# Kernel optimization log

Hardware: AMD Instinct MI355X
Metric: run time of the kernel (lower is better)

The kernel has to match this reference:

```python
import jax, jax.numpy as jnp
import numpy as np

NEG = -10000000.0

def setup_inputs() -> dict:
    key0 = jax.random.key(0)
    ks = jax.random.split(key0, 5)
    B, XL, KL, D = 16, 1024, 512, 1024  # D = 2*rnn_dim
    return {
        "x": jax.random.normal(ks[0], (B, XL, D), dtype=jnp.float32),
        "x_mask": jnp.ones((B, XL), dtype=jnp.float32),
        "key": jax.random.normal(ks[1], (B, KL, D), dtype=jnp.float32),
        "key_mask": jnp.ones((B, KL), dtype=jnp.float32),
        "w_input": jax.random.normal(ks[2], (D,), dtype=jnp.float32) / np.sqrt(D),
        "w_key": jax.random.normal(ks[3], (D,), dtype=jnp.float32) / np.sqrt(D),
        "dot_w": jax.random.normal(ks[4], (D,), dtype=jnp.float32) / np.sqrt(D),
    }

def reference(x, x_mask, key, key_mask, w_input, w_key, dot_w):
    # Trilinear attention score S[b,i,j] = w_in.x_i + w_key.k_j + (x_i*dot_w).k_j
    x_logits = jnp.einsum('bxd,d->bx', x, w_input)      # [B, XL]
    key_logits = jnp.einsum('bkd,d->bk', key, w_key)    # [B, KL]
    S = (x_logits[:, :, None] + key_logits[:, None, :]
         + jnp.einsum('bxd,bkd->bxk', x * dot_w, key))  # [B, XL, KL]

    # x -> key attention with joint mask
    joint_mask = 1.0 - x_mask[:, :, None] * key_mask[:, None, :]
    masked_S = S + joint_mask * NEG
    attn = jax.nn.softmax(masked_S, axis=-1)
    x2key = jnp.einsum('bxk,bkd->bxd', attn, key)       # [B, XL, D]

    # key -> x attention: mask over key dim, max-reduce, masked softmax over x
    km = key_mask[:, None, :]
    S2 = S * km + (1.0 - km) * NEG                      # add_masked_value
    max_s = jnp.max(S2, axis=-1)                        # [B, XL]
    p = jax.nn.softmax(max_s * x_mask, axis=-1) * x_mask  # claf masked_softmax
    p = p / (jnp.sum(p, axis=-1, keepdims=True) + 1e-13)
    key2x = jnp.einsum('bx,bxd->bd', p, x)[:, None, :]  # [B, 1, D], broadcasts

    key2x_full = jnp.broadcast_to(key2x, x.shape)
    return jnp.concatenate([x, x2key, x * x2key, x * key2x_full], axis=-1)
```

## Files before the change

### kernel.cpp

```cpp
#include <hip/hip_runtime.h>
#include <hip/hip_fp16.h>

#define B_ 16
#define XL_ 1024
#define KL_ 512
#define D_ 1024
#define NEGC (-10000000.0f)

typedef _Float16 f16x8 __attribute__((ext_vector_type(8)));
typedef float f32x4 __attribute__((ext_vector_type(4)));
typedef unsigned short u16x8 __attribute__((ext_vector_type(8)));
typedef unsigned short u16x4 __attribute__((ext_vector_type(4)));

__device__ __forceinline__ unsigned short f2h(float f) {
  __half h = __float2half(f);
  return __half_as_ushort(h);
}

__global__ __launch_bounds__(256) void k_build(const float* __restrict__ key,
    const float* __restrict__ w_key, unsigned short* __restrict__ KQ2,
    unsigned short* __restrict__ KV2, float* __restrict__ klog) {
  __shared__ unsigned short tile[64][72];
  int bid = blockIdx.x;
  int b = bid >> 4;
  int ks = (bid >> 1) & 7;
  int dh = bid & 1;
  int tid = threadIdx.x;
  int kr = tid >> 2;
  int cq = tid & 3;
  const float* krow = key + ((size_t)(b * KL_ + ks * 64 + kr)) * D_;
  float klacc = 0.f;
  int dl = tid & 63, g = tid >> 6;

  for (int dt = dh * 8; dt < dh * 8 + 8; ++dt) {
#pragma unroll
    for (int j = 0; j < 4; ++j) {
      int c = dt * 64 + cq * 16 + j * 4;
      f32x4 v = __builtin_nontemporal_load((const f32x4*)(krow + c));
      f32x4 w = *(const f32x4*)(w_key + c);
      klacc += v[0] * w[0] + v[1] * w[1] + v[2] * w[2] + v[3] * w[3];
      u16x4 hv;
      hv[0] = f2h(v[0]); hv[1] = f2h(v[1]); hv[2] = f2h(v[2]); hv[3] = f2h(v[3]);
      *(u16x4*)(&tile[kr][cq * 16 + j * 4]) = hv;
    }
    __syncthreads();
#pragma unroll
    for (int dkc_l = 0; dkc_l < 2; ++dkc_l) {
      u16x8 hv = *(const u16x8*)(&tile[kr][dkc_l * 32 + cq * 8]);
      size_t dst = (((size_t)(b * 8 + ks) * 32 + (dt * 2 + dkc_l)) << 11)
                   + (size_t)(((kr >> 4) & 3) * 512 + (cq * 16 + (kr & 15)) * 8);
      *(u16x8*)(KQ2 + dst) = hv;
    }
    {
      int dglob = dt * 64 + dl;
      int wv_ = dglob >> 7, np = (dglob >> 4) & 7, l15v = dglob & 15;
#pragma unroll
      for (int kkc_l = 0; kkc_l < 2; ++kkc_l) {
        u16x8 hv;
#pragma unroll
        for (int h = 0; h < 8; ++h) hv[h] = tile[kkc_l * 32 + g * 8 + h][dl];
        size_t dst = (((size_t)(b * 8 + wv_) * 16 + (ks * 2 + kkc_l)) << 12)
                     + (size_t)(np * 512 + (g * 16 + l15v) * 8);
        *(u16x8*)(KV2 + dst) = hv;
      }
    }
    __syncthreads();
  }
  klacc += __shfl_xor(klacc, 1);
  klacc += __shfl_xor(klacc, 2);
  if (cq == 0) atomicAdd(&klog[b * KL_ + ks * 64 + kr], klacc);
}

__global__ __launch_bounds__(512, 4) void k_attn(
    const float* __restrict__ x, const float* __restrict__ x_mask,
    const float* __restrict__ key_mask, const float* __restrict__ dot_w,
    const float* __restrict__ w_input,
    const unsigned short* __restrict__ KQ2, const unsigned short* __restrict__ KV2,
    const float* __restrict__ klog,
    float* __restrict__ maxs, float* __restrict__ out) {
  __shared__ unsigned short Qall[32 * 1024];
  __shared__ float xlg[32];
  unsigned short* Pt = Qall;
  float* redA = (float*)(Qall + 16384);
  float* redB = redA + 256;
  float* redC = redB + 256;

  const int tid = threadIdx.x;
  const int wv = tid >> 6;
  const int lane = tid & 63;
  const int l15 = lane & 15, l4 = lane >> 4;
  const int r7 = l15 & 7;

  int bid = blockIdx.x;
  int b = (bid & 7) * 2 + (bid >> 8);
  int x0 = ((bid >> 3) & 31) * 32;

  const float* xB = x + ((size_t)b * XL_ + x0) * D_;

  {
    int row = tid >> 4;
    int cg = tid & 15;
    const float* sp = xB + (size_t)row * D_;
    char* qrow = (char*)Qall + row * 2048;
    int rsw = row & 7;
    float xl = 0.f;
#pragma unroll
    for (int j = 0; j < 16; ++j) {
      int c4 = cg + j * 16;
      f32x4 v = *(const f32x4*)(sp + c4 * 4);
      f32x4 w = *(const f32x4*)(dot_w + c4 * 4);
      f32x4 wi = *(const f32x4*)(w_input + c4 * 4);
      xl += v[0] * wi[0] + v[1] * wi[1] + v[2] * wi[2] + v[3] * wi[3];
      u16x4 hv;
      hv[0] = f2h(v[0] * w[0]); hv[1] = f2h(v[1] * w[1]);
      hv[2] = f2h(v[2] * w[2]); hv[3] = f2h(v[3] * w[3]);
      *(u16x4*)(qrow + (((c4 >> 1) ^ rsw) << 4) + ((c4 & 1) << 3)) = hv;
    }
    xl += __shfl_xor(xl, 1);
    xl += __shfl_xor(xl, 2);
    xl += __shfl_xor(xl, 4);
    xl += __shfl_xor(xl, 8);
    if (cg == 0) xlg[row] = xl;
  }
  __syncthreads();

  f32x4 acc[2][4];
#pragma unroll
  for (int m = 0; m < 2; ++m)
#pragma unroll
    for (int n = 0; n < 4; ++n) { f32x4 z = {0.f, 0.f, 0.f, 0.f}; acc[m][n] = z; }

  const unsigned short* KQ2w = KQ2 + (((size_t)(b * 8 + wv) * 32) << 11) + lane * 8;
  const char* qa0 = (char*)Qall + l15 * 2048;
  const char* qa1 = (char*)Qall + (16 + l15) * 2048;

#pragma unroll 4
  for (int dk = 0; dk < D_; dk += 32) {
    const unsigned short* cp = KQ2w + ((dk >> 5) << 11);
    f16x8 b0 = *(const f16x8*)(cp);
    f16x8 b1 = *(const f16x8*)(cp + 512);
    f16x8 b2 = *(const f16x8*)(cp + 1024);
    f16x8 b3 = *(const f16x8*)(cp + 1536);
    int c = (((dk >> 3) + l4) ^ r7) << 4;
    f16x8 a0 = *(const f16x8*)(qa0 + c);
    f16x8 a1 = *(const f16x8*)(qa1 + c);
    __builtin_amdgcn_s_setprio(1);
    acc[0][0] = __builtin_amdgcn_mfma_f32_16x16x32_f16(b0, a0, acc[0][0], 0, 0, 0);
    acc[1][0] = __builtin_amdgcn_mfma_f32_16x16x32_f16(b0, a1, acc[1][0], 0, 0, 0);
    acc[0][1] = __builtin_amdgcn_mfma_f32_16x16x32_f16(b1, a0, acc[0][1], 0, 0, 0);
    acc[1][1] = __builtin_amdgcn_mfma_f32_16x16x32_f16(b1, a1, acc[1][1], 0, 0, 0);
    acc[0][2] = __builtin_amdgcn_mfma_f32_16x16x32_f16(b2, a0, acc[0][2], 0, 0, 0);
    acc[1][2] = __builtin_amdgcn_mfma_f32_16x16x32_f16(b2, a1, acc[1][2], 0, 0, 0);
    acc[0][3] = __builtin_amdgcn_mfma_f32_16x16x32_f16(b3, a0, acc[0][3], 0, 0, 0);
    acc[1][3] = __builtin_amdgcn_mfma_f32_16x16x32_f16(b3, a1, acc[1][3], 0, 0, 0);
    __builtin_amdgcn_s_setprio(0);
  }
  __syncthreads();

  float xlv[2], xmv[2];
#pragma unroll
  for (int m = 0; m < 2; ++m) {
    int row = m * 16 + l15;
    xlv[m] = xlg[row];
    xmv[m] = x_mask[(size_t)b * XL_ + x0 + row];
  }
  f32x4 klv[4], kmv[4];
#pragma unroll
  for (int n = 0; n < 4; ++n) {
    int kb = wv * 64 + n * 16 + l4 * 4;
    klv[n] = *(const f32x4*)(klog + (size_t)b * KL_ + kb);
    kmv[n] = *(const f32x4*)(key_mask + (size_t)b * KL_ + kb);
  }
  float mxsm[2] = {-3.0e38f, -3.0e38f}, mxs2[2] = {-3.0e38f, -3.0e38f};
#pragma unroll
  for (int m = 0; m < 2; ++m)
#pragma unroll
    for (int n = 0; n < 4; ++n)
#pragma unroll
      for (int q = 0; q < 4; ++q) {
        float s = acc[m][n][q] + xlv[m] + klv[n][q];
        float sm = s + (1.f - xmv[m] * kmv[n][q]) * NEGC;
        float s2 = s * kmv[n][q] + (1.f - kmv[n][q]) * NEGC;
        mxsm[m] = fmaxf(mxsm[m], sm);
        mxs2[m] = fmaxf(mxs2[m], s2);
      }
#pragma unroll
  for (int m = 0; m < 2; ++m) {
    mxsm[m] = fmaxf(mxsm[m], __shfl_xor(mxsm[m], 16));
    mxsm[m] = fmaxf(mxsm[m], __shfl_xor(mxsm[m], 32));
    mxs2[m] = fmaxf(mxs2[m], __shfl_xor(mxs2[m], 16));
    mxs2[m] = fmaxf(mxs2[m], __shfl_xor(mxs2[m], 32));
  }
  if (l4 == 0) {
#pragma unroll
    for (int m = 0; m < 2; ++m) {
      redA[wv * 32 + m * 16 + l15] = mxsm[m];
      redB[wv * 32 + m * 16 + l15] = mxs2[m];
    }
  }
  __syncthreads();
  float gmx[2];
#pragma unroll
  for (int m = 0; m < 2; ++m) {
    int row = m * 16 + l15;
    float v = redA[row];
#pragma unroll
    for (int w = 1; w < 8; ++w) v = fmaxf(v, redA[w * 32 + row]);
    gmx[m] = v;
  }
  if (tid < 32) {
    float v = redB[tid];
#pragma unroll
    for (int w = 1; w < 8; ++w) v = fmaxf(v, redB[w * 32 + tid]);
    maxs[(size_t)b * XL_ + x0 + tid] = v;
  }
  float rs[2] = {0.f, 0.f};
#pragma unroll
  for (int m = 0; m < 2; ++m) {
    int row = m * 16 + l15;
    char* prow = (char*)Pt + row * 1024;
    int rsw = row & 7;
#pragma unroll
    for (int n = 0; n < 4; ++n) {
      int k = wv * 64 + n * 16 + l4 * 4;
      u16x4 pk;
#pragma unroll
      for (int q = 0; q < 4; ++q) {
        float s = acc[m][n][q] + xlv[m] + klv[n][q];
        float sm = s + (1.f - xmv[m] * kmv[n][q]) * NEGC;
        float e = __expf(sm - gmx[m]);
        rs[m] += e;
        pk[q] = f2h(e);
      }
      *(u16x4*)(prow + ((((k >> 3) ^ rsw) << 4) + ((k & 4) << 1))) = pk;
    }
  }
#pragma unroll
  for (int m = 0; m < 2; ++m) {
    rs[m] += __shfl_xor(rs[m], 16);
    rs[m] += __shfl_xor(rs[m], 32);
  }
  if (l4 == 0) {
#pragma unroll
    for (int m = 0; m < 2; ++m) redC[wv * 32 + m * 16 + l15] = rs[m];
  }
  __syncthreads();

  float dn[2];
#pragma unroll
  for (int m = 0; m < 2; ++m) {
    int row = m * 16 + l15;
    float sum = redC[row];
#pragma unroll
    for (int w = 1; w < 8; ++w) sum += redC[w * 32 + row];
    dn[m] = 1.f / sum;
  }
  size_t obase0 = ((size_t)b * XL_ + x0) * (size_t)(4 * D_);
  const char* pa0 = (char*)Pt + l15 * 1024;
  const char* pa1 = (char*)Pt + (16 + l15) * 1024;
  const unsigned short* KV2w = KV2 + (((size_t)(b * 8 + wv) * 16) << 12) + lane * 8;
#pragma unroll
  for (int sc = 0; sc < 2; ++sc) {
    int c0 = wv * 128 + sc * 64;
    f32x4 acc2[2][4];
#pragma unroll
    for (int m = 0; m < 2; ++m)
#pragma unroll
      for (int n = 0; n < 4; ++n) { f32x4 z = {0.f, 0.f, 0.f, 0.f}; acc2[m][n] = z; }
    const unsigned short* KV2s = KV2w + sc * 4 * 512;
#pragma unroll 4
    for (int kk = 0; kk < KL_; kk += 32) {
      const unsigned short* cp = KV2s + ((kk >> 5) << 12);
      f16x8 b0 = *(const f16x8*)(cp);
      f16x8 b1 = *(const f16x8*)(cp + 512);
      f16x8 b2 = *(const f16x8*)(cp + 1024);
      f16x8 b3 = *(const f16x8*)(cp + 1536);
      int c = ((((kk >> 3) + l4) ^ r7) << 4);
      f16x8 a0 = *(const f16x8*)(pa0 + c);
      f16x8 a1 = *(const f16x8*)(pa1 + c);
      __builtin_amdgcn_s_setprio(1);
      acc2[0][0] = __builtin_amdgcn_mfma_f32_16x16x32_f16(b0, a0, acc2[0][0], 0, 0, 0);
      acc2[1][0] = __builtin_amdgcn_mfma_f32_16x16x32_f16(b0, a1, acc2[1][0], 0, 0, 0);
      acc2[0][1] = __builtin_amdgcn_mfma_f32_16x16x32_f16(b1, a0, acc2[0][1], 0, 0, 0);
      acc2[1][1] = __builtin_amdgcn_mfma_f32_16x16x32_f16(b1, a1, acc2[1][1], 0, 0, 0);
      acc2[0][2] = __builtin_amdgcn_mfma_f32_16x16x32_f16(b2, a0, acc2[0][2], 0, 0, 0);
      acc2[1][2] = __builtin_amdgcn_mfma_f32_16x16x32_f16(b2, a1, acc2[1][2], 0, 0, 0);
      acc2[0][3] = __builtin_amdgcn_mfma_f32_16x16x32_f16(b3, a0, acc2[0][3], 0, 0, 0);
      acc2[1][3] = __builtin_amdgcn_mfma_f32_16x16x32_f16(b3, a1, acc2[1][3], 0, 0, 0);
      __builtin_amdgcn_s_setprio(0);
    }
#pragma unroll
    for (int m = 0; m < 2; ++m) {
      int row = m * 16 + l15;
      size_t ob = obase0 + (size_t)row * (4 * D_);
#pragma unroll
      for (int n = 0; n < 4; ++n) {
        int col = c0 + n * 16 + l4 * 4;
        f32x4 v = acc2[m][n];
        v[0] *= dn[m]; v[1] *= dn[m]; v[2] *= dn[m]; v[3] *= dn[m];
        __builtin_nontemporal_store(v, (f32x4*)(out + ob + D_ + col));
      }
    }
  }
}

__global__ __launch_bounds__(256) void k_key2x_part(const float* __restrict__ x,
    const float* __restrict__ maxs, const float* __restrict__ x_mask,
    float* __restrict__ partial) {
  int b = blockIdx.x >> 4;
  int xc = blockIdx.x & 15;
  int tid = threadIdx.x;
  int wvi = tid >> 6, lane = tid & 63;
  __shared__ float r1[4], r2[4], r3[4];
  __shared__ float ps_all[XL_];
  const float* ms = maxs + (size_t)b * XL_;
  const float* xm = x_mask + (size_t)b * XL_;
  float tv[4], xmv[4];
  float vmax = -3.0e38f;
#pragma unroll
  for (int i = 0; i < 4; ++i) {
    int xi = i * 256 + tid;
    xmv[i] = xm[xi];
    tv[i] = ms[xi] * xmv[i];
    vmax = fmaxf(vmax, tv[i]);
  }
#pragma unroll
  for (int sh = 32; sh >= 1; sh >>= 1) vmax = fmaxf(vmax, __shfl_xor(vmax, sh));
  if (lane == 0) r1[wvi] = vmax;
  __syncthreads();
  float gmax = fmaxf(fmaxf(r1[0], r1[1]), fmaxf(r1[2], r1[3]));
  float e[4]; float es = 0.f;
#pragma unroll
  for (int i = 0; i < 4; ++i) { e[i] = __expf(tv[i] - gmax); es += e[i]; }
#pragma unroll
  for (int sh = 32; sh >= 1; sh >>= 1) es += __shfl_xor(es, sh);
  if (lane == 0) r2[wvi] = es;
  __syncthreads();
  float gsum = r2[0] + r2[1] + r2[2] + r2[3];
  float pv4[4]; float psum = 0.f;
#pragma unroll
  for (int i = 0; i < 4; ++i) { pv4[i] = e[i] / gsum * xmv[i]; psum += pv4[i]; }
#pragma unroll
  for (int sh = 32; sh >= 1; sh >>= 1) psum += __shfl_xor(psum, sh);
  if (lane == 0) r3[wvi] = psum;
  __syncthreads();
  float gps = r3[0] + r3[1] + r3[2] + r3[3];
  float inv = 1.f / (gps + 1e-13f);
#pragma unroll
  for (int i = 0; i < 4; ++i) ps_all[i * 256 + tid] = pv4[i] * inv;
  __syncthreads();
  const float* xb = x + ((size_t)b * XL_ + xc * 64) * D_;
  float acc0 = 0.f, acc1 = 0.f, acc2 = 0.f, acc3 = 0.f;
  int d = tid;
  const float* psl = ps_all + xc * 64;
  for (int xi = 0; xi < 64; ++xi) {
    float pv = psl[xi];
    const float* rp = xb + (size_t)xi * D_;
    acc0 += pv * __builtin_nontemporal_load(rp + d);
    acc1 += pv * __builtin_nontemporal_load(rp + d + 256);
    acc2 += pv * __builtin_nontemporal_load(rp + d + 512);
    acc3 += pv * __builtin_nontemporal_load(rp + d + 768);
  }
  float* pp = partial + (size_t)blockIdx.x * D_;
  pp[d] = acc0; pp[d + 256] = acc1; pp[d + 512] = acc2; pp[d + 768] = acc3;
}

__global__ __launch_bounds__(256) void k_key2x_red(const float* __restrict__ partial,
    float* __restrict__ k2x) {
  int idx = blockIdx.x * 256 + threadIdx.x;
  int b = idx >> 10;
  float s = 0.f;
#pragma unroll
  for (int xc = 0; xc < 16; ++xc)
    s += partial[((size_t)b * 16 + xc) * D_ + (idx & 1023)];
  k2x[idx] = s;
}

__global__ __launch_bounds__(256) void k_mega(const float* __restrict__ x,
    const float* __restrict__ k2x, float* __restrict__ out) {
  size_t t = (size_t)blockIdx.x * 256 + threadIdx.x;
  size_t base = t * 4;
  int b = (int)(base >> 20);
  int rem = (int)(base & ((1u << 20) - 1));
  int xr = rem >> 10;
  int d = rem & 1023;
  f32x4 xv = __builtin_nontemporal_load((const f32x4*)(x + base));
  f32x4 kv = *(const f32x4*)(k2x + (size_t)b * D_ + d);
  float* orow = out + ((size_t)b * XL_ + xr) * (size_t)(4 * D_);
  f32x4 x2 = __builtin_nontemporal_load((const f32x4*)(orow + D_ + d));
  __builtin_nontemporal_store(xv, (f32x4*)(orow + d));
  f32x4 p2;
  p2[0] = xv[0] * x2[0]; p2[1] = xv[1] * x2[1];
  p2[2] = xv[2] * x2[2]; p2[3] = xv[3] * x2[3];
  __builtin_nontemporal_store(p2, (f32x4*)(orow + 2 * D_ + d));
  f32x4 p3;
  p3[0] = xv[0] * kv[0]; p3[1] = xv[1] * kv[1];
  p3[2] = xv[2] * kv[2]; p3[3] = xv[3] * kv[3];
  __builtin_nontemporal_store(p3, (f32x4*)(orow + 3 * D_ + d));
}

extern "C" void kernel_launch(void* const* d_in, const int* in_sizes, int n_in,
                              void* d_out, int out_size, void* d_ws, size_t ws_size,
                              hipStream_t stream) {
  (void)in_sizes; (void)n_in; (void)out_size; (void)ws_size;
  const float* x        = (const float*)d_in[0];
  const float* x_mask   = (const float*)d_in[1];
  const float* key      = (const float*)d_in[2];
  const float* key_mask = (const float*)d_in[3];
  const float* w_input  = (const float*)d_in[4];
  const float* w_key    = (const float*)d_in[5];
  const float* dot_w    = (const float*)d_in[6];
  float* out = (float*)d_out;
  char* ws = (char*)d_ws;

  unsigned short* KQ2 = (unsigned short*)ws;
  unsigned short* KV2 = (unsigned short*)(ws + (16u << 20));
  float* xlog = (float*)(ws + (32u << 20));
  float* klog = xlog + B_ * XL_;
  float* maxs = klog + B_ * KL_;
  float* pbuf = maxs + B_ * XL_;
  float* k2x  = pbuf + B_ * XL_;
  float* partial = (float*)ws;

  hipMemsetAsync(klog, 0, B_ * KL_ * sizeof(float), stream);
  k_build<<<dim3(B_ * 16), dim3(256), 0, stream>>>(key, w_key, KQ2, KV2, klog);
  k_attn<<<dim3(512), dim3(512), 0, stream>>>(x, x_mask, key_mask, dot_w, w_input,
                                              KQ2, KV2, klog, maxs, out);
  k_key2x_part<<<dim3(B_ * 16), dim3(256), 0, stream>>>(x, maxs, x_mask, partial);
  k_key2x_red<<<dim3(B_ * D_ / 256), dim3(256), 0, stream>>>(partial, k2x);
  k_mega<<<dim3(B_ * XL_ * D_ / 1024), dim3(256), 0, stream>>>(x, k2x, out);
}
```

Measured before the change: 169.1 us.

## Prefetch MFMA B-operands in registers and drop klog memset via partial sums

The QK and PV MFMA loops now double-buffer their global B-operand loads in registers, fetching the next 64-wide step while the current one computes. The first KQ2 and KV2 tiles are prefetched before the Q staging and the softmax epilogue, so their latency overlaps that work. k_build now splits D into four quarters across twice as many blocks and writes per-quarter key logits instead of using atomics. That removes the memset launch, and k_attn sums the four partials. The cost is higher register pressure under launch_bounds(512,4) and some extra klog reads.

```diff
diff --git a/kernel.cpp b/kernel.cpp
--- a/kernel.cpp
+++ b/kernel.cpp
@@ -19,12 +19,12 @@
 
 __global__ __launch_bounds__(256) void k_build(const float* __restrict__ key,
     const float* __restrict__ w_key, unsigned short* __restrict__ KQ2,
-    unsigned short* __restrict__ KV2, float* __restrict__ klog) {
+    unsigned short* __restrict__ KV2, float* __restrict__ klogP) {
   __shared__ unsigned short tile[64][72];
   int bid = blockIdx.x;
-  int b = bid >> 4;
-  int ks = (bid >> 1) & 7;
-  int dh = bid & 1;
+  int b = bid >> 5;
+  int ks = (bid >> 2) & 7;
+  int dq = bid & 3;
   int tid = threadIdx.x;
   int kr = tid >> 2;
   int cq = tid & 3;
@@ -32,7 +32,7 @@
   float klacc = 0.f;
   int dl = tid & 63, g = tid >> 6;
 
-  for (int dt = dh * 8; dt < dh * 8 + 8; ++dt) {
+  for (int dt = dq * 4; dt < dq * 4 + 4; ++dt) {
 #pragma unroll
     for (int j = 0; j < 4; ++j) {
       int c = dt * 64 + cq * 16 + j * 4;
@@ -68,7 +68,7 @@
   }
   klacc += __shfl_xor(klacc, 1);
   klacc += __shfl_xor(klacc, 2);
-  if (cq == 0) atomicAdd(&klog[b * KL_ + ks * 64 + kr], klacc);
+  if (cq == 0) klogP[(size_t)dq * (B_ * KL_) + b * KL_ + ks * 64 + kr] = klacc;
 }
 
 __global__ __launch_bounds__(512, 4) void k_attn(
@@ -76,7 +76,7 @@
     const float* __restrict__ key_mask, const float* __restrict__ dot_w,
     const float* __restrict__ w_input,
     const unsigned short* __restrict__ KQ2, const unsigned short* __restrict__ KV2,
-    const float* __restrict__ klog,
+    const float* __restrict__ klogP,
     float* __restrict__ maxs, float* __restrict__ out) {
   __shared__ unsigned short Qall[32 * 1024];
   __shared__ float xlg[32];
@@ -96,6 +96,16 @@
   int x0 = ((bid >> 3) & 31) * 32;
 
   const float* xB = x + ((size_t)b * XL_ + x0) * D_;
+  const unsigned short* KQ2w = KQ2 + (((size_t)(b * 8 + wv) * 32) << 11) + lane * 8;
+
+  f16x8 p00 = *(const f16x8*)(KQ2w);
+  f16x8 p01 = *(const f16x8*)(KQ2w + 512);
+  f16x8 p02 = *(const f16x8*)(KQ2w + 1024);
+  f16x8 p03 = *(const f16x8*)(KQ2w + 1536);
+  f16x8 p10 = *(const f16x8*)(KQ2w + 2048);
+  f16x8 p11 = *(const f16x8*)(KQ2w + 2048 + 512);
+  f16x8 p12 = *(const f16x8*)(KQ2w + 2048 + 1024);
+  f16x8 p13 = *(const f16x8*)(KQ2w + 2048 + 1536);
 
   {
     int row = tid >> 4;
@@ -130,32 +140,66 @@
 #pragma unroll
     for (int n = 0; n < 4; ++n) { f32x4 z = {0.f, 0.f, 0.f, 0.f}; acc[m][n] = z; }
 
-  const unsigned short* KQ2w = KQ2 + (((size_t)(b * 8 + wv) * 32) << 11) + lane * 8;
   const char* qa0 = (char*)Qall + l15 * 2048;
   const char* qa1 = (char*)Qall + (16 + l15) * 2048;
 
-#pragma unroll 4
-  for (int dk = 0; dk < D_; dk += 32) {
-    const unsigned short* cp = KQ2w + ((dk >> 5) << 11);
-    f16x8 b0 = *(const f16x8*)(cp);
-    f16x8 b1 = *(const f16x8*)(cp + 512);
-    f16x8 b2 = *(const f16x8*)(cp + 1024);
-    f16x8 b3 = *(const f16x8*)(cp + 1536);
-    int c = (((dk >> 3) + l4) ^ r7) << 4;
-    f16x8 a0 = *(const f16x8*)(qa0 + c);
-    f16x8 a1 = *(const f16x8*)(qa1 + c);
-    __builtin_amdgcn_s_setprio(1);
-    acc[0][0] = __builtin_amdgcn_mfma_f32_16x16x32_f16(b0, a0, acc[0][0], 0, 0, 0);
-    acc[1][0] = __builtin_amdgcn_mfma_f32_16x16x32_f16(b0, a1, acc[1][0], 0, 0, 0);
-    acc[0][1] = __builtin_amdgcn_mfma_f32_16x16x32_f16(b1, a0, acc[0][1], 0, 0, 0);
-    acc[1][1] = __builtin_amdgcn_mfma_f32_16x16x32_f16(b1, a1, acc[1][1], 0, 0, 0);
-    acc[0][2] = __builtin_amdgcn_mfma_f32_16x16x32_f16(b2, a0, acc[0][2], 0, 0, 0);
-    acc[1][2] = __builtin_amdgcn_mfma_f32_16x16x32_f16(b2, a1, acc[1][2], 0, 0, 0);
-    acc[0][3] = __builtin_amdgcn_mfma_f32_16x16x32_f16(b3, a0, acc[0][3], 0, 0, 0);
-    acc[1][3] = __builtin_amdgcn_mfma_f32_16x16x32_f16(b3, a1, acc[1][3], 0, 0, 0);
-    __builtin_amdgcn_s_setprio(0);
-  }
-  __syncthreads();
+#pragma unroll 2
+  for (int dk = 0; dk < D_; dk += 64) {
+    {
+      f16x8 b0 = p00, b1 = p01, b2 = p02, b3 = p03;
+      if (dk + 64 < D_) {
+        const unsigned short* cp = KQ2w + (((dk + 64) >> 5) << 11);
+        p00 = *(const f16x8*)(cp);
+        p01 = *(const f16x8*)(cp + 512);
+        p02 = *(const f16x8*)(cp + 1024);
+        p03 = *(const f16x8*)(cp + 1536);
+      }
+      int c = (((dk >> 3) + l4) ^ r7) << 4;
+      f16x8 a0 = *(const f16x8*)(qa0 + c);
+      f16x8 a1 = *(const f16x8*)(qa1 + c);
+      __builtin_amdgcn_s_setprio(1);
+      acc[0][0] = __builtin_amdgcn_mfma_f32_16x16x32_f16(b0, a0, acc[0][0], 0, 0, 0);
+      acc[1][0] = __builtin_amdgcn_mfma_f32_16x16x32_f16(b0, a1, acc[1][0], 0, 0, 0);
+      acc[0][1] = __builtin_amdgcn_mfma_f32_16x16x32_f16(b1, a0, acc[0][1], 0, 0, 0);
+      acc[1][1] = __builtin_amdgcn_mfma_f32_16x16x32_f16(b1, a1, acc[1][1], 0, 0, 0);
+      acc[0][2] = __builtin_amdgcn_mfma_f32_16x16x32_f16(b2, a0, acc[0][2], 0, 0, 0);
+      acc[1][2] = __builtin_amdgcn_mfma_f32_16x16x32_f16(b2, a1, acc[1][2], 0, 0, 0);
+      acc[0][3] = __builtin_amdgcn_mfma_f32_16x16x32_f16(b3, a0, acc[0][3], 0, 0, 0);
+      acc[1][3] = __builtin_amdgcn_mfma_f32_16x16x32_f16(b3, a1, acc[1][3], 0, 0, 0);
+      __builtin_amdgcn_s_setprio(0);
+    }
+    {
+      int dk2 = dk + 32;
+      f16x8 b0 = p10, b1 = p11, b2 = p12, b3 = p13;
+      if (dk2 + 64 < D_) {
+        const unsigned short* cp = KQ2w + (((dk2 + 64) >> 5) << 11);
+        p10 = *(const f16x8*)(cp);
+        p11 = *(const f16x8*)(cp + 512);
+        p12 = *(const f16x8*)(cp + 1024);
+        p13 = *(const f16x8*)(cp + 1536);
+      }
+      int c = (((dk2 >> 3) + l4) ^ r7) << 4;
+      f16x8 a0 = *(const f16x8*)(qa0 + c);
+      f16x8 a1 = *(const f16x8*)(qa1 + c);
+      __builtin_amdgcn_s_setprio(1);
+      acc[0][0] = __builtin_amdgcn_mfma_f32_16x16x32_f16(b0, a0, acc[0][0], 0, 0, 0);
+      acc[1][0] = __builtin_amdgcn_mfma_f32_16x16x32_f16(b0, a1, acc[1][0], 0, 0, 0);
+      acc[0][1] = __builtin_amdgcn_mfma_f32_16x16x32_f16(b1, a0, acc[0][1], 0, 0, 0);
+      acc[1][1] = __builtin_amdgcn_mfma_f32_16x16x32_f16(b1, a1, acc[1][1], 0, 0, 0);
+      acc[0][2] = __builtin_amdgcn_mfma_f32_16x16x32_f16(b2, a0, acc[0][2], 0, 0, 0);
+      acc[1][2] = __builtin_amdgcn_mfma_f32_16x16x32_f16(b2, a1, acc[1][2], 0, 0, 0);
+      acc[0][3] = __builtin_amdgcn_mfma_f32_16x16x32_f16(b3, a0, acc[0][3], 0, 0, 0);
+      acc[1][3] = __builtin_amdgcn_mfma_f32_16x16x32_f16(b3, a1, acc[1][3], 0, 0, 0);
+      __builtin_amdgcn_s_setprio(0);
+    }
+  }
+  __syncthreads();
+
+  const unsigned short* KV2w = KV2 + (((size_t)(b * 8 + wv) * 16) << 12) + lane * 8;
+  f16x8 v00 = *(const f16x8*)(KV2w);
+  f16x8 v01 = *(const f16x8*)(KV2w + 512);
+  f16x8 v02 = *(const f16x8*)(KV2w + 1024);
+  f16x8 v03 = *(const f16x8*)(KV2w + 1536);
 
   float xlv[2], xmv[2];
 #pragma unroll
@@ -168,7 +212,11 @@
 #pragma unroll
   for (int n = 0; n < 4; ++n) {
     int kb = wv * 64 + n * 16 + l4 * 4;
-    klv[n] = *(const f32x4*)(klog + (size_t)b * KL_ + kb);
+    f32x4 s0 = *(const f32x4*)(klogP + (size_t)b * KL_ + kb);
+    f32x4 s1 = *(const f32x4*)(klogP + (size_t)(B_ * KL_) + (size_t)b * KL_ + kb);
+    f32x4 s2 = *(const f32x4*)(klogP + (size_t)(2 * B_ * KL_) + (size_t)b * KL_ + kb);
+    f32x4 s3 = *(const f32x4*)(klogP + (size_t)(3 * B_ * KL_) + (size_t)b * KL_ + kb);
+    klv[n] = (s0 + s1) + (s2 + s3);
     kmv[n] = *(const f32x4*)(key_mask + (size_t)b * KL_ + kb);
   }
   float mxsm[2] = {-3.0e38f, -3.0e38f}, mxs2[2] = {-3.0e38f, -3.0e38f};
@@ -258,7 +306,6 @@
   size_t obase0 = ((size_t)b * XL_ + x0) * (size_t)(4 * D_);
   const char* pa0 = (char*)Pt + l15 * 1024;
   const char* pa1 = (char*)Pt + (16 + l15) * 1024;
-  const unsigned short* KV2w = KV2 + (((size_t)(b * 8 + wv) * 16) << 12) + lane * 8;
 #pragma unroll
   for (int sc = 0; sc < 2; ++sc) {
     int c0 = wv * 128 + sc * 64;
@@ -268,26 +315,67 @@
 #pragma unroll
       for (int n = 0; n < 4; ++n) { f32x4 z = {0.f, 0.f, 0.f, 0.f}; acc2[m][n] = z; }
     const unsigned short* KV2s = KV2w + sc * 4 * 512;
-#pragma unroll 4
-    for (int kk = 0; kk < KL_; kk += 32) {
-      const unsigned short* cp = KV2s + ((kk >> 5) << 12);
-      f16x8 b0 = *(const f16x8*)(cp);
-      f16x8 b1 = *(const f16x8*)(cp + 512);
-      f16x8 b2 = *(const f16x8*)(cp + 1024);
-      f16x8 b3 = *(const f16x8*)(cp + 1536);
-      int c = ((((kk >> 3) + l4) ^ r7) << 4);
-      f16x8 a0 = *(const f16x8*)(pa0 + c);
-      f16x8 a1 = *(const f16x8*)(pa1 + c);
-      __builtin_amdgcn_s_setprio(1);
-      acc2[0][0] = __builtin_amdgcn_mfma_f32_16x16x32_f16(b0, a0, acc2[0][0], 0, 0, 0);
-      acc2[1][0] = __builtin_amdgcn_mfma_f32_16x16x32_f16(b0, a1, acc2[1][0], 0, 0, 0);
-      acc2[0][1] = __builtin_amdgcn_mfma_f32_16x16x32_f16(b1, a0, acc2[0][1], 0, 0, 0);
-      acc2[1][1] = __builtin_amdgcn_mfma_f32_16x16x32_f16(b1, a1, acc2[1][1], 0, 0, 0);
-      acc2[0][2] = __builtin_amdgcn_mfma_f32_16x16x32_f16(b2, a0, acc2[0][2], 0, 0, 0);
-      acc2[1][2] = __builtin_amdgcn_mfma_f32_16x16x32_f16(b2, a1, acc2[1][2], 0, 0, 0);
-      acc2[0][3] = __builtin_amdgcn_mfma_f32_16x16x32_f16(b3, a0, acc2[0][3], 0, 0, 0);
-      acc2[1][3] = __builtin_amdgcn_mfma_f32_16x16x32_f16(b3, a1, acc2[1][3], 0, 0, 0);
-      __builtin_amdgcn_s_setprio(0);
+    f16x8 q00, q01, q02, q03, q10, q11, q12, q13;
+    if (sc == 0) { q00 = v00; q01 = v01; q02 = v02; q03 = v03; }
+    else {
+      q00 = *(const f16x8*)(KV2s);
+      q01 = *(const f16x8*)(KV2s + 512);
+      q02 = *(const f16x8*)(KV2s + 1024);
+      q03 = *(const f16x8*)(KV2s + 1536);
+    }
+    q10 = *(const f16x8*)(KV2s + 4096);
+    q11 = *(const f16x8*)(KV2s + 4096 + 512);
+    q12 = *(const f16x8*)(KV2s + 4096 + 1024);
+    q13 = *(const f16x8*)(KV2s + 4096 + 1536);
+#pragma unroll 2
+    for (int kk = 0; kk < KL_; kk += 64) {
+      {
+        f16x8 b0 = q00, b1 = q01, b2 = q02, b3 = q03;
+        if (kk + 64 < KL_) {
+          const unsigned short* cp = KV2s + (((kk + 64) >> 5) << 12);
+          q00 = *(const f16x8*)(cp);
+          q01 = *(const f16x8*)(cp + 512);
+          q02 = *(const f16x8*)(cp + 1024);
+          q03 = *(const f16x8*)(cp + 1536);
+        }
+        int c = ((((kk >> 3) + l4) ^ r7) << 4);
+        f16x8 a0 = *(const f16x8*)(pa0 + c);
+        f16x8 a1 = *(const f16x8*)(pa1 + c);
+        __builtin_amdgcn_s_setprio(1);
+        acc2[0][0] = __builtin_amdgcn_mfma_f32_16x16x32_f16(b0, a0, acc2[0][0], 0, 0, 0);
+        acc2[1][0] = __builtin_amdgcn_mfma_f32_16x16x32_f16(b0, a1, acc2[1][0], 0, 0, 0);
+        acc2[0][1] = __builtin_amdgcn_mfma_f32_16x16x32_f16(b1, a0, acc2[0][1], 0, 0, 0);
+        acc2[1][1] = __builtin_amdgcn_mfma_f32_16x16x32_f16(b1, a1, acc2[1][1], 0, 0, 0);
+        acc2[0][2] = __builtin_amdgcn_mfma_f32_16x16x32_f16(b2, a0, acc2[0][2], 0, 0, 0);
+        acc2[1][2] = __builtin_amdgcn_mfma_f32_16x16x32_f16(b2, a1, acc2[1][2], 0, 0, 0);
+        acc2[0][3] = __builtin_amdgcn_mfma_f32_16x16x32_f16(b3, a0, acc2[0][3], 0, 0, 0);
+        acc2[1][3] = __builtin_amdgcn_mfma_f32_16x16x32_f16(b3, a1, acc2[1][3], 0, 0, 0);
+        __builtin_amdgcn_s_setprio(0);
+      }
+      {
+        int kk2 = kk + 32;
+        f16x8 b0 = q10, b1 = q11, b2 = q12, b3 = q13;
+        if (kk2 + 64 < KL_) {
+          const unsigned short* cp = KV2s + (((kk2 + 64) >> 5) << 12);
+          q10 = *(const f16x8*)(cp);
+          q11 = *(const f16x8*)(cp + 512);
+          q12 = *(const f16x8*)(cp + 1024);
+          q13 = *(const f16x8*)(cp + 1536);
+        }
+        int c = ((((kk2 >> 3) + l4) ^ r7) << 4);
+        f16x8 a0 = *(const f16x8*)(pa0 + c);
+        f16x8 a1 = *(const f16x8*)(pa1 + c);
+        __builtin_amdgcn_s_setprio(1);
+        acc2[0][0] = __builtin_amdgcn_mfma_f32_16x16x32_f16(b0, a0, acc2[0][0], 0, 0, 0);
+        acc2[1][0] = __builtin_amdgcn_mfma_f32_16x16x32_f16(b0, a1, acc2[1][0], 0, 0, 0);
+        acc2[0][1] = __builtin_amdgcn_mfma_f32_16x16x32_f16(b1, a0, acc2[0][1], 0, 0, 0);
+        acc2[1][1] = __builtin_amdgcn_mfma_f32_16x16x32_f16(b1, a1, acc2[1][1], 0, 0, 0);
+        acc2[0][2] = __builtin_amdgcn_mfma_f32_16x16x32_f16(b2, a0, acc2[0][2], 0, 0, 0);
+        acc2[1][2] = __builtin_amdgcn_mfma_f32_16x16x32_f16(b2, a1, acc2[1][2], 0, 0, 0);
+        acc2[0][3] = __builtin_amdgcn_mfma_f32_16x16x32_f16(b3, a0, acc2[0][3], 0, 0, 0);
+        acc2[1][3] = __builtin_amdgcn_mfma_f32_16x16x32_f16(b3, a1, acc2[1][3], 0, 0, 0);
+        __builtin_amdgcn_s_setprio(0);
+      }
     }
 #pragma unroll
     for (int m = 0; m < 2; ++m) {
@@ -415,17 +503,14 @@
 
   unsigned short* KQ2 = (unsigned short*)ws;
   unsigned short* KV2 = (unsigned short*)(ws + (16u << 20));
-  float* xlog = (float*)(ws + (32u << 20));
-  float* klog = xlog + B_ * XL_;
-  float* maxs = klog + B_ * KL_;
-  float* pbuf = maxs + B_ * XL_;
-  float* k2x  = pbuf + B_ * XL_;
+  float* klogP = (float*)(ws + (32u << 20));
+  float* maxs = klogP + 4 * B_ * KL_;
+  float* k2x  = maxs + B_ * XL_;
   float* partial = (float*)ws;
 
-  hipMemsetAsync(klog, 0, B_ * KL_ * sizeof(float), stream);
-  k_build<<<dim3(B_ * 16), dim3(256), 0, stream>>>(key, w_key, KQ2, KV2, klog);
+  k_build<<<dim3(B_ * 32), dim3(256), 0, stream>>>(key, w_key, KQ2, KV2, klogP);
   k_attn<<<dim3(512), dim3(512), 0, stream>>>(x, x_mask, key_mask, dot_w, w_input,
-                                              KQ2, KV2, klog, maxs, out);
+                                              KQ2, KV2, klogP, maxs, out);
   k_key2x_part<<<dim3(B_ * 16), dim3(256), 0, stream>>>(x, maxs, x_mask, partial);
   k_key2x_red<<<dim3(B_ * D_ / 256), dim3(256), 0, stream>>>(partial, k2x);
   k_mega<<<dim3(B_ * XL_ * D_ / 1024), dim3(256), 0, stream>>>(x, k2x, out);
```

Measured after the change: 163.0 us (median of 2 runs). 3.6% less time.
